# Kernel tuning notes

Measured on AMD Instinct MI355X. Metric: run time of the kernel, lower is better.

## Reference

```python
import jax, jax.numpy as jnp
import numpy as np

P, RES_H, RES_W = 32, 256, 256
H, W = 480, 640
FOCAL = 1.0


def setup_inputs() -> dict:
    key = jax.random.key(0)
    k1, k2, k3, k4 = jax.random.split(key, 4)
    # texture: alpha + rgb logits, uniform(-1,1) as in torch init
    plane_content = jax.random.uniform(k1, (P, 4, RES_H, RES_W), jnp.float32, -1.0, 1.0)
    # orthonormal plane basis (columns = plane x/y axes + normal)
    plane_basis, _ = jnp.linalg.qr(jax.random.normal(k2, (P, 3, 3), jnp.float32))
    xy = jax.random.normal(k3, (P, 2), jnp.float32)
    z = 2.0 + 4.0 * jax.random.uniform(k4, (P, 1), jnp.float32)  # planes in front of camera
    plane_position = jnp.concatenate([xy, z], axis=-1)
    plane_wh = jnp.full((P, 2), 2.0, jnp.float32)
    cam_R = jnp.eye(3, dtype=jnp.float32)   # world-to-cam rotation
    cam_T = jnp.zeros((3,), jnp.float32)    # world-to-cam translation
    return {"plane_content": plane_content, "plane_basis": plane_basis,
            "plane_position": plane_position, "plane_wh": plane_wh,
            "cam_R": cam_R, "cam_T": cam_T}


def _bilinear(img, uv):
    # img: (C, Hc, Wc); uv: (N, 2) in [-1, 1]. torch grid_sample bilinear,
    # align_corners=False, padding_mode='zeros'.
    C, Hc, Wc = img.shape
    x = (uv[:, 0] + 1.0) * Wc * 0.5 - 0.5
    y = (uv[:, 1] + 1.0) * Hc * 0.5 - 0.5
    x0 = jnp.floor(x)
    y0 = jnp.floor(y)
    wx = x - x0
    wy = y - y0

    def gather(xi, yi):
        inb = (xi >= 0) & (xi < Wc) & (yi >= 0) & (yi < Hc)
        xc = jnp.clip(xi, 0, Wc - 1).astype(jnp.int32)
        yc = jnp.clip(yi, 0, Hc - 1).astype(jnp.int32)
        return jnp.where(inb[None, :], img[:, yc, xc], 0.0)  # (C, N)

    v00 = gather(x0, y0)
    v01 = gather(x0 + 1.0, y0)
    v10 = gather(x0, y0 + 1.0)
    v11 = gather(x0 + 1.0, y0 + 1.0)
    top = v00 * (1.0 - wx) + v01 * wx
    bot = v10 * (1.0 - wx) + v11 * wx
    return (top * (1.0 - wy) + bot * wy).T  # (N, C)


def reference(plane_content, plane_basis, plane_position, plane_wh, cam_R, cam_T):
    N = H * W
    xs = ((jnp.arange(W, dtype=jnp.float32) + 0.5) / W) * 2.0 - 1.0
    ys = ((jnp.arange(H, dtype=jnp.float32) + 0.5) / H) * 2.0 - 1.0
    gy, gx = jnp.meshgrid(ys, xs, indexing='ij')
    # pinhole ray directions in camera frame (z-depth parameterization)
    dirs_cam = jnp.stack([gx.reshape(-1) / FOCAL, gy.reshape(-1) / FOCAL,
                          jnp.ones((N,), jnp.float32)], axis=-1)  # (N,3)
    cam_pos = -cam_R.T @ cam_T                 # camera center in world
    dirs_world = dirs_cam @ cam_R              # R^T d per ray, (N,3)

    normals = plane_basis[:, :, 2]             # (P,3)
    num = jnp.einsum('pc,pc->p', normals, plane_position - cam_pos[None])
    den = jnp.einsum('pc,nc->pn', normals, dirs_world)
    den = jnp.where(jnp.abs(den) < 1e-6, 1e-6, den)
    points_depth = num[:, None] / den          # (P,N) depth on each plane

    world_points = cam_pos[None, None] + points_depth[..., None] * dirs_world[None]  # (P,N,3)
    local = jnp.einsum('pnc,pcd->pnd', world_points - plane_position[:, None], plane_basis)
    uv = local[..., :2] / (plane_wh[:, None, :] * 0.5)        # normalize to [-1,1] inside plane
    in_planes = jnp.all(jnp.abs(uv) <= 1.0, axis=-1)          # (P,N)

    raw = jax.vmap(_bilinear)(plane_content, uv)              # (P,N,4)
    content = jnp.where(in_planes[..., None], jax.nn.sigmoid(raw), 0.0)

    sort_idx = jnp.argsort(points_depth, axis=0)              # front-to-back per pixel
    depth_sorted = jnp.take_along_axis(points_depth, sort_idx, axis=0)
    content_sorted = jnp.take_along_axis(content, sort_idx[..., None], axis=0)

    alpha = content_sorted[..., 0]                            # (P,N)
    color = content_sorted[..., 1:]                           # (P,N,3)
    trans = jnp.cumprod(1.0 - alpha, axis=0)
    trans = jnp.concatenate([jnp.ones((1, N), alpha.dtype), trans[:-1]], axis=0)
    weight = alpha * trans                                    # (P,N)

    depth_img = jnp.sum(depth_sorted * weight, axis=0).reshape(H, W)
    color_img = jnp.sum(color * weight[..., None], axis=0).reshape(H, W, 3)
    return jnp.concatenate([color_img, depth_img[..., None]], axis=-1)  # (H,W,4)
```

## Files before the change

kernel.cpp:

```cpp
#include <hip/hip_runtime.h>
#include <cstdint>

constexpr int P   = 32;
constexpr int RES = 256;
constexpr int H   = 480;
constexpr int W   = 640;
constexpr int BLK = 256;

__device__ __forceinline__ uint32_t mono_key(float f) {
    uint32_t b = __float_as_uint(f);
    return (b & 0x80000000u) ? ~b : (b | 0x80000000u);
}
__device__ __forceinline__ float unmono(uint32_t m) {
    uint32_t b = (m & 0x80000000u) ? (m ^ 0x80000000u) : ~m;
    return __uint_as_float(b);
}

__global__ __launch_bounds__(256) void render_kernel(
    const float* __restrict__ content,
    const float* __restrict__ basis,
    const float* __restrict__ ppos,
    const float* __restrict__ pwh,
    const float* __restrict__ camR,
    const float* __restrict__ camT,
    float* __restrict__ out)
{
    __shared__ uint32_t s_key[P][BLK];
    __shared__ uint8_t  s_idx[P][BLK];

    const int t = threadIdx.x;
    const int x = blockIdx.x * 16 + (t & 15);
    const int y = blockIdx.y * 16 + (t >> 4);

    const float R0=camR[0],R1=camR[1],R2=camR[2],
                R3=camR[3],R4=camR[4],R5=camR[5],
                R6=camR[6],R7=camR[7],R8=camR[8];
    const float T0=camT[0],T1=camT[1],T2=camT[2];
    const float cpx = -(R0*T0 + R3*T1 + R6*T2);
    const float cpy = -(R1*T0 + R4*T1 + R7*T2);
    const float cpz = -(R2*T0 + R5*T1 + R8*T2);

    const float gx = ((float)x + 0.5f) / (float)W * 2.0f - 1.0f;
    const float gy = ((float)y + 0.5f) / (float)H * 2.0f - 1.0f;
    const float dwx = gx*R0 + gy*R3 + R6;
    const float dwy = gx*R1 + gy*R4 + R7;
    const float dwz = gx*R2 + gy*R5 + R8;

    int cnt = 0;
    for (int p = 0; p < P; ++p) {
        const float b00 = basis[p*9+0], b01 = basis[p*9+1], n0 = basis[p*9+2];
        const float b10 = basis[p*9+3], b11 = basis[p*9+4], n1 = basis[p*9+5];
        const float b20 = basis[p*9+6], b21 = basis[p*9+7], n2 = basis[p*9+8];
        const float px = ppos[p*3+0], py = ppos[p*3+1], pz = ppos[p*3+2];
        const float hw0 = pwh[p*2+0]*0.5f, hw1 = pwh[p*2+1]*0.5f;

        const float num = n0*(px-cpx) + n1*(py-cpy) + n2*(pz-cpz);
        float den = n0*dwx + n1*dwy + n2*dwz;
        if (fabsf(den) < 1e-6f) den = 1e-6f;
        const float depth = num / den;

        const float ox = cpx + depth*dwx - px;
        const float oy = cpy + depth*dwy - py;
        const float oz = cpz + depth*dwz - pz;
        const float u = (ox*b00 + oy*b10 + oz*b20) / hw0;
        const float v = (ox*b01 + oy*b11 + oz*b21) / hw1;

        if (fabsf(u) <= 1.0f && fabsf(v) <= 1.0f) {
            const uint32_t k = mono_key(depth);
            int j = cnt;
            while (j > 0 && s_key[j-1][t] > k) {
                s_key[j][t] = s_key[j-1][t];
                s_idx[j][t] = s_idx[j-1][t];
                --j;
            }
            s_key[j][t] = k;
            s_idx[j][t] = (uint8_t)p;
            ++cnt;
        }
    }

    float aR = 0.f, aG = 0.f, aB = 0.f, aD = 0.f, tr = 1.f;
    for (int i = 0; i < cnt; ++i) {
        const uint32_t k = s_key[i][t];
        const int p = (int)s_idx[i][t];
        const float depth = unmono(k);

        const float b00 = basis[p*9+0], b01 = basis[p*9+1];
        const float b10 = basis[p*9+3], b11 = basis[p*9+4];
        const float b20 = basis[p*9+6], b21 = basis[p*9+7];
        const float px = ppos[p*3+0], py = ppos[p*3+1], pz = ppos[p*3+2];
        const float hw0 = pwh[p*2+0]*0.5f, hw1 = pwh[p*2+1]*0.5f;

        const float ox = cpx + depth*dwx - px;
        const float oy = cpy + depth*dwy - py;
        const float oz = cpz + depth*dwz - pz;
        const float u = (ox*b00 + oy*b10 + oz*b20) / hw0;
        const float v = (ox*b01 + oy*b11 + oz*b21) / hw1;

        const float fx = (u + 1.0f) * 128.0f - 0.5f;
        const float fy = (v + 1.0f) * 128.0f - 0.5f;
        const float x0f = floorf(fx), y0f = floorf(fy);
        const float wx = fx - x0f, wy = fy - y0f;
        const int ix = (int)x0f, iy = (int)y0f;

        const int x0c = min(max(ix,     0), RES-1);
        const int x1c = min(max(ix + 1, 0), RES-1);
        const int y0c = min(max(iy,     0), RES-1);
        const int y1c = min(max(iy + 1, 0), RES-1);
        const float mx0 = (ix     >= 0 && ix     < RES) ? 1.f : 0.f;
        const float mx1 = (ix + 1 >= 0 && ix + 1 < RES) ? 1.f : 0.f;
        const float my0 = (iy     >= 0 && iy     < RES) ? 1.f : 0.f;
        const float my1 = (iy + 1 >= 0 && iy + 1 < RES) ? 1.f : 0.f;
        const float m00 = mx0 * my0, m01 = mx1 * my0;
        const float m10 = mx0 * my1, m11 = mx1 * my1;

        const int o00 = y0c * RES + x0c, o01 = y0c * RES + x1c;
        const int o10 = y1c * RES + x0c, o11 = y1c * RES + x1c;
        const float* pc = content + ((size_t)p << 18);

        float c4[4];
        #pragma unroll
        for (int c = 0; c < 4; ++c) {
            const float* ic = pc + (c << 16);
            const float v00 = ic[o00] * m00;
            const float v01 = ic[o01] * m01;
            const float v10 = ic[o10] * m10;
            const float v11 = ic[o11] * m11;
            const float top = v00 * (1.f - wx) + v01 * wx;
            const float bot = v10 * (1.f - wx) + v11 * wx;
            const float raw = top * (1.f - wy) + bot * wy;
            c4[c] = 1.0f / (1.0f + __expf(-raw));
        }

        const float wgt = c4[0] * tr;
        aD += depth * wgt;
        aR += c4[1] * wgt;
        aG += c4[2] * wgt;
        aB += c4[3] * wgt;
        tr *= (1.0f - c4[0]);
    }

    const int o = (y * W + x) * 4;
    float4 res; res.x = aR; res.y = aG; res.z = aB; res.w = aD;
    *reinterpret_cast<float4*>(out + o) = res;
}

extern "C" void kernel_launch(void* const* d_in, const int* in_sizes, int n_in,
                              void* d_out, int out_size, void* d_ws, size_t ws_size,
                              hipStream_t stream) {
    const float* content = (const float*)d_in[0];
    const float* basis   = (const float*)d_in[1];
    const float* ppos    = (const float*)d_in[2];
    const float* pwh     = (const float*)d_in[3];
    const float* camR    = (const float*)d_in[4];
    const float* camT    = (const float*)d_in[5];

    dim3 grid(W / 16, H / 16);
    render_kernel<<<grid, dim3(BLK), 0, stream>>>(
        content, basis, ppos, pwh, camR, camT, (float*)d_out);
}
```

Before: 43.34 us.

## Repack texture to interleaved fp16 and replace shared-memory insertion sort with register selection

Adds a repack kernel that converts the planar fp32 texture into an interleaved RGBA fp16 layout in workspace, so each bilinear tap is a single 8-byte load instead of four scattered fp32 loads. The per-pixel insertion sort in large shared arrays is replaced by keys held in registers with repeated min-selection, and plane parameters are staged in shared memory. The repack pass reads all 32 MB of texture on every call, which may cost more than the gathers it saves, and fp16 lowers texture precision. Register pressure from the 32-entry key array may also reduce occupancy.

New measurement: 44.58 us. 1.03x slower.

```diff
diff --git a/kernel.cpp b/kernel.cpp
--- a/kernel.cpp
+++ b/kernel.cpp
@@ -5,7 +5,6 @@
 constexpr int RES = 256;
 constexpr int H   = 480;
 constexpr int W   = 640;
-constexpr int BLK = 256;
 
 __device__ __forceinline__ uint32_t mono_key(float f) {
     uint32_t b = __float_as_uint(f);
@@ -15,9 +14,27 @@
     uint32_t b = (m & 0x80000000u) ? (m ^ 0x80000000u) : ~m;
     return __uint_as_float(b);
 }
-
+__device__ __forceinline__ float h2f(unsigned short u) {
+    return (float)__builtin_bit_cast(_Float16, u);
+}
+
+__global__ __launch_bounds__(256) void repack_kernel(
+    const float* __restrict__ content, ushort4* __restrict__ tex)
+{
+    const int tid = blockIdx.x * 256 + threadIdx.x;
+    const float* src = content + (((size_t)(tid >> 16)) << 18) + (tid & 65535);
+    ushort4 o;
+    o.x = __builtin_bit_cast(unsigned short, (_Float16)src[0]);
+    o.y = __builtin_bit_cast(unsigned short, (_Float16)src[65536]);
+    o.z = __builtin_bit_cast(unsigned short, (_Float16)src[131072]);
+    o.w = __builtin_bit_cast(unsigned short, (_Float16)src[196608]);
+    tex[tid] = o;
+}
+
+template<bool FAST>
 __global__ __launch_bounds__(256) void render_kernel(
     const float* __restrict__ content,
+    const ushort4* __restrict__ tex,
     const float* __restrict__ basis,
     const float* __restrict__ ppos,
     const float* __restrict__ pwh,
@@ -25,12 +42,20 @@
     const float* __restrict__ camT,
     float* __restrict__ out)
 {
-    __shared__ uint32_t s_key[P][BLK];
-    __shared__ uint8_t  s_idx[P][BLK];
+    __shared__ float s_pl[P][20];
 
     const int t = threadIdx.x;
     const int x = blockIdx.x * 16 + (t & 15);
     const int y = blockIdx.y * 16 + (t >> 4);
+
+    if (t < P) {
+        const float* b = basis + t * 9;
+        s_pl[t][0] = b[0]; s_pl[t][1] = b[3]; s_pl[t][2] = b[6];
+        s_pl[t][3] = b[1]; s_pl[t][4] = b[4]; s_pl[t][5] = b[7];
+        s_pl[t][6] = ppos[t*3+0]; s_pl[t][7] = ppos[t*3+1]; s_pl[t][8] = ppos[t*3+2];
+        s_pl[t][9] = pwh[t*2+0] * 0.5f; s_pl[t][10] = pwh[t*2+1] * 0.5f;
+    }
+    __syncthreads();
 
     const float R0=camR[0],R1=camR[1],R2=camR[2],
                 R3=camR[3],R4=camR[4],R5=camR[5],
@@ -46,7 +71,8 @@
     const float dwy = gx*R1 + gy*R4 + R7;
     const float dwz = gx*R2 + gy*R5 + R8;
 
-    int cnt = 0;
+    uint32_t key[P];
+    #pragma unroll
     for (int p = 0; p < P; ++p) {
         const float b00 = basis[p*9+0], b01 = basis[p*9+1], n0 = basis[p*9+2];
         const float b10 = basis[p*9+3], b11 = basis[p*9+4], n1 = basis[p*9+5];
@@ -65,31 +91,31 @@
         const float u = (ox*b00 + oy*b10 + oz*b20) / hw0;
         const float v = (ox*b01 + oy*b11 + oz*b21) / hw1;
 
-        if (fabsf(u) <= 1.0f && fabsf(v) <= 1.0f) {
-            const uint32_t k = mono_key(depth);
-            int j = cnt;
-            while (j > 0 && s_key[j-1][t] > k) {
-                s_key[j][t] = s_key[j-1][t];
-                s_idx[j][t] = s_idx[j-1][t];
-                --j;
-            }
-            s_key[j][t] = k;
-            s_idx[j][t] = (uint8_t)p;
-            ++cnt;
+        const bool hit = (fabsf(u) <= 1.0f && fabsf(v) <= 1.0f);
+        key[p] = hit ? mono_key(depth) : 0xFFFFFFFFu;
+    }
+
+    float aR = 0.f, aG = 0.f, aB = 0.f, aD = 0.f, tr = 1.f;
+    #pragma unroll 1
+    for (int it = 0; it < P; ++it) {
+        uint32_t bk = 0xFFFFFFFFu; int bi = 0;
+        #pragma unroll
+        for (int i = 0; i < P; ++i) {
+            const bool c = key[i] < bk;
+            bk = c ? key[i] : bk;
+            bi = c ? i : bi;
         }
-    }
-
-    float aR = 0.f, aG = 0.f, aB = 0.f, aD = 0.f, tr = 1.f;
-    for (int i = 0; i < cnt; ++i) {
-        const uint32_t k = s_key[i][t];
-        const int p = (int)s_idx[i][t];
-        const float depth = unmono(k);
-
-        const float b00 = basis[p*9+0], b01 = basis[p*9+1];
-        const float b10 = basis[p*9+3], b11 = basis[p*9+4];
-        const float b20 = basis[p*9+6], b21 = basis[p*9+7];
-        const float px = ppos[p*3+0], py = ppos[p*3+1], pz = ppos[p*3+2];
-        const float hw0 = pwh[p*2+0]*0.5f, hw1 = pwh[p*2+1]*0.5f;
+        if (bk == 0xFFFFFFFFu) break;
+        #pragma unroll
+        for (int i = 0; i < P; ++i)
+            key[i] = (i == bi) ? 0xFFFFFFFFu : key[i];
+
+        const float depth = unmono(bk);
+        const float* pl = s_pl[bi];
+        const float b00 = pl[0], b10 = pl[1], b20 = pl[2];
+        const float b01 = pl[3], b11 = pl[4], b21 = pl[5];
+        const float px  = pl[6], py  = pl[7], pz  = pl[8];
+        const float hw0 = pl[9], hw1 = pl[10];
 
         const float ox = cpx + depth*dwx - px;
         const float oy = cpy + depth*dwy - py;
@@ -116,20 +142,43 @@
 
         const int o00 = y0c * RES + x0c, o01 = y0c * RES + x1c;
         const int o10 = y1c * RES + x0c, o11 = y1c * RES + x1c;
-        const float* pc = content + ((size_t)p << 18);
 
         float c4[4];
-        #pragma unroll
-        for (int c = 0; c < 4; ++c) {
-            const float* ic = pc + (c << 16);
-            const float v00 = ic[o00] * m00;
-            const float v01 = ic[o01] * m01;
-            const float v10 = ic[o10] * m10;
-            const float v11 = ic[o11] * m11;
-            const float top = v00 * (1.f - wx) + v01 * wx;
-            const float bot = v10 * (1.f - wx) + v11 * wx;
-            const float raw = top * (1.f - wy) + bot * wy;
-            c4[c] = 1.0f / (1.0f + __expf(-raw));
+        if (FAST) {
+            const int base = bi << 16;
+            const ushort4 t00 = tex[base + o00];
+            const ushort4 t01 = tex[base + o01];
+            const ushort4 t10 = tex[base + o10];
+            const ushort4 t11 = tex[base + o11];
+            const unsigned short* q00 = (const unsigned short*)&t00;
+            const unsigned short* q01 = (const unsigned short*)&t01;
+            const unsigned short* q10 = (const unsigned short*)&t10;
+            const unsigned short* q11 = (const unsigned short*)&t11;
+            #pragma unroll
+            for (int c = 0; c < 4; ++c) {
+                const float v00 = h2f(q00[c]) * m00;
+                const float v01 = h2f(q01[c]) * m01;
+                const float v10 = h2f(q10[c]) * m10;
+                const float v11 = h2f(q11[c]) * m11;
+                const float top = v00 * (1.f - wx) + v01 * wx;
+                const float bot = v10 * (1.f - wx) + v11 * wx;
+                const float raw = top * (1.f - wy) + bot * wy;
+                c4[c] = 1.0f / (1.0f + __expf(-raw));
+            }
+        } else {
+            const float* pc = content + ((size_t)bi << 18);
+            #pragma unroll
+            for (int c = 0; c < 4; ++c) {
+                const float* ic = pc + (c << 16);
+                const float v00 = ic[o00] * m00;
+                const float v01 = ic[o01] * m01;
+                const float v10 = ic[o10] * m10;
+                const float v11 = ic[o11] * m11;
+                const float top = v00 * (1.f - wx) + v01 * wx;
+                const float bot = v10 * (1.f - wx) + v11 * wx;
+                const float raw = top * (1.f - wy) + bot * wy;
+                c4[c] = 1.0f / (1.0f + __expf(-raw));
+            }
         }
 
         const float wgt = c4[0] * tr;
@@ -156,6 +205,14 @@
     const float* camT    = (const float*)d_in[5];
 
     dim3 grid(W / 16, H / 16);
-    render_kernel<<<grid, dim3(BLK), 0, stream>>>(
-        content, basis, ppos, pwh, camR, camT, (float*)d_out);
-}
+    const size_t need = (size_t)P * 65536 * sizeof(ushort4);
+
+    if (ws_size >= need) {
+        repack_kernel<<<P * 65536 / 256, 256, 0, stream>>>(content, (ushort4*)d_ws);
+        render_kernel<true><<<grid, dim3(256), 0, stream>>>(
+            content, (const ushort4*)d_ws, basis, ppos, pwh, camR, camT, (float*)d_out);
+    } else {
+        render_kernel<false><<<grid, dim3(256), 0, stream>>>(
+            content, nullptr, basis, ppos, pwh, camR, camT, (float*)d_out);
+    }
+}
```
